# Optimization experiments

Measured on AMD Instinct MI355X. Metric: run time of the kernel, lower is better.

The kernel has to match this reference:

```python
import jax, jax.numpy as jnp
import numpy as np

N = 384       # nodes
K = 60        # neighbors per node
SUB = 20      # subsample_k
C_S = 128
C_Z = 128
H = 4
D_HEAD = C_Z // H
NUM_RBF = 64
E = N * K
EPS = 1e-8


def _rbf(D, D_min=0.0, D_max=20.0, D_count=NUM_RBF):
    # radial basis expansion of distances: [..., ] -> [..., D_count]
    mu = jnp.linspace(D_min, D_max, D_count)
    sigma = (D_max - D_min) / D_count
    return jnp.exp(-(((D[..., None] - mu) / sigma) ** 2))


def setup_inputs() -> dict:
    key = jax.random.key(0)
    ks = jax.random.split(key, 16)
    f32 = jnp.float32
    inp = {
        "node_features": jax.random.normal(ks[0], (N, C_S), f32),
        "node_trans": jax.random.normal(ks[1], (N, 3), f32) * 5.0,
        "edge_features": jax.random.normal(ks[2], (E, C_Z), f32),
        "edge_index": jax.random.randint(ks[3], (2, E), 0, N),
        "subsample_idx": jax.random.randint(ks[4], (N, K, SUB), 0, K),
        # dist_bias_gate: Linear(2*c_s -> H)
        "W_gate": jax.random.normal(ks[5], (2 * C_S, H), f32) / np.sqrt(2 * C_S),
        "b_gate": jnp.zeros((H,), f32),
        # dist_bias: Linear(num_rbf -> H)
        "W_db": jax.random.normal(ks[6], (NUM_RBF, H), f32) / np.sqrt(NUM_RBF),
        "b_db": jnp.zeros((H,), f32),
        # lin_qk: Linear(c_z -> 2*c_z)
        "W_qk": jax.random.normal(ks[7], (C_Z, 2 * C_Z), f32) / np.sqrt(C_Z),
        "b_qk": jnp.zeros((2 * C_Z,), f32),
        # lin_v: Linear(c_z -> c_z)
        "W_v": jax.random.normal(ks[8], (C_Z, C_Z), f32) / np.sqrt(C_Z),
        "b_v": jnp.zeros((C_Z,), f32),
        # lin_out: Linear(c_z -> c_z) (init='final' in source; random here for testing)
        "W_out": jax.random.normal(ks[9], (C_Z, C_Z), f32) / np.sqrt(C_Z),
        "b_out": jnp.zeros((C_Z,), f32),
    }
    return inp


def reference(node_features, node_trans, edge_features, edge_index, subsample_idx,
              W_gate, b_gate, W_db, b_db, W_qk, b_qk, W_v, b_v, W_out, b_out):
    n, k, sub = subsample_idx.shape
    # assume_sorted=True path: edges are grouped k-per-destination-node
    dst = edge_index[0].reshape(n, k)                           # [n,k] neighbor ids
    edge1 = jnp.broadcast_to(dst[:, :, None], (n, k, sub))      # [n,k,sub]
    edge2 = jnp.take_along_axis(
        jnp.broadcast_to(dst[:, None, :], (n, k, k)), subsample_idx, axis=-1)  # [n,k,sub]

    f1 = node_features[edge1]                                   # [n,k,sub,c_s]
    f2 = node_features[edge2]
    gate = jax.nn.sigmoid(jnp.concatenate([f1, f2], axis=-1) @ W_gate + b_gate)  # [n,k,sub,H]

    t1 = node_trans[edge1]                                      # [n,k,sub,3]
    t2 = node_trans[edge2]
    dist = jnp.linalg.norm(t1 - t2 + EPS, axis=-1)              # [n,k,sub]
    bias = gate * (_rbf(dist) @ W_db + b_db)                    # [n,k,sub,H]

    edges = edge_features.reshape(n, k, C_Z)
    qk = edges @ W_qk + b_qk
    q, kk = jnp.split(qk, 2, axis=-1)
    q = q.reshape(n, k, H, D_HEAD)
    kk = kk.reshape(n, k, H, D_HEAD)

    batch = jnp.arange(n)[:, None, None]
    k_sub = kk[batch, subsample_idx]                            # [n,k,sub,H,d]
    attn = jnp.einsum('nkhd,nkshd->nksh', q, k_sub) / np.sqrt(C_Z) + bias
    attn = jax.nn.softmax(attn, axis=2)                         # softmax over subsample axis

    v = (edges @ W_v + b_v).reshape(n, k, H, D_HEAD)
    v_sub = v[batch, subsample_idx]                             # [n,k,sub,H,d]
    upd = jnp.einsum('nksh,nkshd->nkhd', attn, v_sub).reshape(n * k, C_Z)
    return upd @ W_out + b_out                                  # [E, c_z]
```

## Files before the change

### kernel.cpp

```cpp
#include <hip/hip_runtime.h>
#include <hip/hip_bf16.h>

typedef unsigned short ushortT;
typedef __attribute__((ext_vector_type(8))) short bf16x8;
typedef __attribute__((ext_vector_type(4))) float f32x4;

#define N_NODES 384
#define KNBR 60
#define SUBK 20
#define NEDGE (N_NODES * KNBR)
#define EPSC 1e-8f
#define INV_SQRT_CZ 0.08838834764831845f
#define MU_STEP (20.0f / 63.0f)
#define INV_MU_STEP (63.0f / 20.0f)
#define INV_SIGMA 3.2f

__device__ __forceinline__ float bflo(unsigned int u) { return __uint_as_float(u << 16); }
__device__ __forceinline__ float bfhi(unsigned int u) { return __uint_as_float(u & 0xffff0000u); }
__device__ __forceinline__ ushortT f2bu(float v) {
  union { float f; unsigned int u; } c;
  c.f = v;
  return (ushortT)((c.u + 0x7fffu + ((c.u >> 16) & 1u)) >> 16);
}
__device__ __forceinline__ unsigned int pack2bf(float x, float y) {
  return (unsigned int)f2bu(x) | ((unsigned int)f2bu(y) << 16);
}
__device__ __forceinline__ ushortT f2h(float x) {
  _Float16 h = (_Float16)x;
  return __builtin_bit_cast(ushortT, h);
}
__device__ __forceinline__ float h2f(ushortT u) {
  return (float)__builtin_bit_cast(_Float16, u);
}

__global__ __launch_bounds__(256) void prep_kernel(
    const float* __restrict__ nf, const float* __restrict__ Wg, float* __restrict__ g,
    const float* __restrict__ Wqk, const float* __restrict__ bqk,
    const float* __restrict__ Wv, const float* __restrict__ bv,
    const float* __restrict__ Wout,
    ushortT* __restrict__ Wp1, ushortT* __restrict__ Wp2, float* __restrict__ bc) {
  int b = blockIdx.x, tid = threadIdx.x;
  if (b < 96) {
    int n = b * 4 + (tid >> 6), t = tid & 63;
    float a = nf[n * 128 + t];
    float bb = nf[n * 128 + 64 + t];
    float acc[8];
#pragma unroll
    for (int h = 0; h < 4; ++h) {
      acc[h]     = a * Wg[t * 4 + h]         + bb * Wg[(t + 64) * 4 + h];
      acc[4 + h] = a * Wg[(128 + t) * 4 + h] + bb * Wg[(192 + t) * 4 + h];
    }
#pragma unroll
    for (int i = 0; i < 8; ++i)
#pragma unroll
      for (int off = 32; off >= 1; off >>= 1) acc[i] += __shfl_xor(acc[i], off, 64);
    if (t == 0) {
#pragma unroll
      for (int i = 0; i < 8; ++i) g[n * 8 + i] = acc[i];
    }
  } else {
    int i = (b - 96) * 256 + tid;
    if (i < 49152) {
      int j = i & 7, l = (i >> 3) & 63, t = (i >> 9) & 3;
      int nt = (i >> 11) % 12, ny = (i >> 11) / 12;
      int nn = ny * 192 + nt * 16 + (l & 15);
      int k = t * 32 + (l >> 4) * 8 + j;
      float v = (nn < 256) ? Wqk[k * 256 + nn] : Wv[k * 128 + (nn - 256)];
      Wp1[i] = f2bu(v);
    } else {
      int i2 = i - 49152;
      int j = i2 & 7, l = (i2 >> 3) & 63, t = (i2 >> 9) & 3, nt = (i2 >> 11);
      int nn = nt * 16 + (l & 15);
      int k = t * 32 + (l >> 4) * 8 + j;
      Wp2[i2] = f2bu(Wout[k * 128 + nn]);
    }
    if (i < 384) bc[i] = (i < 256) ? bqk[i] : bv[i - 256];
  }
}

__global__ __launch_bounds__(256) void fused_kernel(
    const float* __restrict__ ef, const ushortT* __restrict__ Wp1,
    const ushortT* __restrict__ Wp2, const float* __restrict__ bc,
    const float* __restrict__ bout, const float* __restrict__ g,
    const float* __restrict__ node_trans, const int* __restrict__ edge_index,
    const int* __restrict__ sub_idx, const float* __restrict__ W_db,
    const float* __restrict__ b_db, const float* __restrict__ b_gate,
    float* __restrict__ outp) {
  __shared__ __align__(16) ushortT kvb[KNBR * 256];
  __shared__ __align__(16) ushortT updq[64 * 136];
  __shared__ __align__(16) ushortT unionb[4800];
  __shared__ ushortT sub_lds[KNBR * SUBK];
  __shared__ float trs[KNBR * 3];
  __shared__ float gg[KNBR * 8];
  __shared__ __align__(16) float wdb_lds[256];

  int n = blockIdx.x, tid = threadIdx.x;
  int e0 = n * KNBR;
  int w = tid >> 6, l = tid & 63;
  int lr = l & 15, lc = l >> 4;
  int row = w * 16 + lr;
  int rowc = min(row, KNBR - 1);

  wdb_lds[tid] = W_db[tid];
  if (tid < KNBR) {
    int dst = edge_index[e0 + tid];
#pragma unroll
    for (int c = 0; c < 3; ++c) trs[tid * 3 + c] = node_trans[dst * 3 + c];
#pragma unroll
    for (int i = 0; i < 8; ++i) gg[tid * 8 + i] = g[dst * 8 + i];
  }
  bf16x8 afrag[4];
#pragma unroll
  for (int t = 0; t < 4; ++t) {
    const float* ap = ef + (size_t)(e0 + rowc) * 128 + t * 32 + lc * 8;
    float4 lo = *(const float4*)ap;
    float4 hi = *(const float4*)(ap + 4);
    bf16x8 a;
    a[0] = (short)f2bu(lo.x); a[1] = (short)f2bu(lo.y);
    a[2] = (short)f2bu(lo.z); a[3] = (short)f2bu(lo.w);
    a[4] = (short)f2bu(hi.x); a[5] = (short)f2bu(hi.y);
    a[6] = (short)f2bu(hi.z); a[7] = (short)f2bu(hi.w);
    afrag[t] = a;
  }

  ushortT* Bb0 = unionb;
  ushortT* Bb1 = unionb + 2048;
  {
    uint4 p = *(const uint4*)(Wp1 + tid * 8);
    *(uint4*)(Bb0 + tid * 8) = p;
  }
  __syncthreads();

  float qv[32];
#pragma unroll
  for (int T = 0; T < 24; ++T) {
    if (T < 23) {
      uint4 p = *(const uint4*)(Wp1 + (T + 1) * 2048 + tid * 8);
      *(uint4*)(((T & 1) ? Bb0 : Bb1) + tid * 8) = p;
    }
    const ushortT* bb = (T & 1) ? Bb1 : Bb0;
    f32x4 acc = {0.f, 0.f, 0.f, 0.f};
#pragma unroll
    for (int t = 0; t < 4; ++t) {
      bf16x8 bfrag = *(const bf16x8*)(bb + (t * 64 + l) * 8);
      acc = __builtin_amdgcn_mfma_f32_16x16x32_bf16(bfrag, afrag[t], acc, 0, 0, 0);
    }
    int col0 = T * 16 + lc * 4;
    float4 bi = *(const float4*)(bc + col0);
    if (T < 8) {
      qv[T * 4 + 0] = (acc[0] + bi.x) * INV_SQRT_CZ;
      qv[T * 4 + 1] = (acc[1] + bi.y) * INV_SQRT_CZ;
      qv[T * 4 + 2] = (acc[2] + bi.z) * INV_SQRT_CZ;
      qv[T * 4 + 3] = (acc[3] + bi.w) * INV_SQRT_CZ;
    } else if (row < KNBR) {
      uint2 o;
      o.x = pack2bf(acc[0] + bi.x, acc[1] + bi.y);
      o.y = pack2bf(acc[2] + bi.z, acc[3] + bi.w);
      int byteoff = ((col0 - 128) * 2) ^ ((row & 7) << 4);
      *(uint2*)((char*)kvb + row * 512 + byteoff) = o;
    }
    __syncthreads();
  }
#pragma unroll
  for (int t = 0; t < 8; ++t) {
    uint2 o;
    o.x = pack2bf(qv[t * 4 + 0], qv[t * 4 + 1]);
    o.y = pack2bf(qv[t * 4 + 2], qv[t * 4 + 3]);
    *(uint2*)(updq + row * 136 + t * 16 + lc * 4) = o;
  }

  ushortT* biasb = unionb;
  float4 bgv = *(const float4*)b_gate;
  float4 bdbv = *(const float4*)b_db;
  for (int p = tid; p < KNBR * SUBK; p += 256) {
    int kl = p / SUBK, s = p - kl * SUBK;
    int j = sub_idx[(size_t)(e0 + kl) * SUBK + s];
    sub_lds[p] = (ushortT)j;
    float dx = trs[kl * 3 + 0] - trs[j * 3 + 0] + EPSC;
    float dy = trs[kl * 3 + 1] - trs[j * 3 + 1] + EPSC;
    float dz = trs[kl * 3 + 2] - trs[j * 3 + 2] + EPSC;
    float dist = sqrtf(dx * dx + dy * dy + dz * dz);
    int r0 = (int)(dist * INV_MU_STEP + 0.5f);
    int rlo = max(r0 - 4, 0), rhi = min(r0 + 4, 63);
    float a0 = 0.f, a1 = 0.f, a2 = 0.f, a3 = 0.f;
    for (int r = rlo; r <= rhi; ++r) {
      float t = (dist - r * MU_STEP) * INV_SIGMA;
      float e = __expf(-t * t);
      float4 wv = ((const float4*)wdb_lds)[r];
      a0 += e * wv.x; a1 += e * wv.y; a2 += e * wv.z; a3 += e * wv.w;
    }
    float g1 = gg[kl * 8 + 0] + gg[j * 8 + 4 + 0] + bgv.x;
    float g2 = gg[kl * 8 + 1] + gg[j * 8 + 4 + 1] + bgv.y;
    float g3 = gg[kl * 8 + 2] + gg[j * 8 + 4 + 2] + bgv.z;
    float g4 = gg[kl * 8 + 3] + gg[j * 8 + 4 + 3] + bgv.w;
    biasb[p * 4 + 0] = f2h((a0 + bdbv.x) / (1.0f + __expf(-g1)));
    biasb[p * 4 + 1] = f2h((a1 + bdbv.y) / (1.0f + __expf(-g2)));
    biasb[p * 4 + 2] = f2h((a2 + bdbv.z) / (1.0f + __expf(-g3)));
    biasb[p * 4 + 3] = f2h((a3 + bdbv.w) / (1.0f + __expf(-g4)));
  }
  __syncthreads();

  const char* kvbase = (const char*)kvb;
  float qh[32];
#pragma unroll
  for (int c = 0; c < 4; ++c) {
    uint4 u = *(const uint4*)(updq + row * 136 + lc * 32 + c * 8);
    qh[c * 8 + 0] = bflo(u.x); qh[c * 8 + 1] = bfhi(u.x);
    qh[c * 8 + 2] = bflo(u.y); qh[c * 8 + 3] = bfhi(u.y);
    qh[c * 8 + 4] = bflo(u.z); qh[c * 8 + 5] = bfhi(u.z);
    qh[c * 8 + 6] = bflo(u.w); qh[c * 8 + 7] = bfhi(u.w);
  }
  float logit[SUBK];
#pragma unroll
  for (int s = 0; s < SUBK; ++s) {
    int j = sub_lds[rowc * SUBK + s];
    int sw = (j & 7) << 4;
    float dot = 0.f;
#pragma unroll
    for (int c = 0; c < 4; ++c) {
      uint4 u = *(const uint4*)(kvbase + j * 512 + ((lc * 64 + c * 16) ^ sw));
      dot += qh[c * 8 + 0] * bflo(u.x) + qh[c * 8 + 1] * bfhi(u.x) +
             qh[c * 8 + 2] * bflo(u.y) + qh[c * 8 + 3] * bfhi(u.y) +
             qh[c * 8 + 4] * bflo(u.z) + qh[c * 8 + 5] * bfhi(u.z) +
             qh[c * 8 + 6] * bflo(u.w) + qh[c * 8 + 7] * bfhi(u.w);
    }
    logit[s] = dot + h2f(biasb[(rowc * SUBK + s) * 4 + lc]);
  }
  float m = logit[0];
#pragma unroll
  for (int s = 1; s < SUBK; ++s) m = fmaxf(m, logit[s]);
  float den = 0.f;
#pragma unroll
  for (int s = 0; s < SUBK; ++s) {
    logit[s] = __expf(logit[s] - m);
    den += logit[s];
  }
  float inv = 1.0f / den;
  float vacc[32];
#pragma unroll
  for (int i = 0; i < 32; ++i) vacc[i] = 0.f;
#pragma unroll
  for (int s = 0; s < SUBK; ++s) {
    int j = sub_lds[rowc * SUBK + s];
    int sw = (j & 7) << 4;
    float wgt = logit[s];
#pragma unroll
    for (int c = 0; c < 4; ++c) {
      uint4 u = *(const uint4*)(kvbase + j * 512 + ((256 + lc * 64 + c * 16) ^ sw));
      vacc[c * 8 + 0] += wgt * bflo(u.x); vacc[c * 8 + 1] += wgt * bfhi(u.x);
      vacc[c * 8 + 2] += wgt * bflo(u.y); vacc[c * 8 + 3] += wgt * bfhi(u.y);
      vacc[c * 8 + 4] += wgt * bflo(u.z); vacc[c * 8 + 5] += wgt * bfhi(u.z);
      vacc[c * 8 + 6] += wgt * bflo(u.w); vacc[c * 8 + 7] += wgt * bfhi(u.w);
    }
  }
#pragma unroll
  for (int c = 0; c < 4; ++c) {
    uint4 o;
    o.x = pack2bf(vacc[c * 8 + 0] * inv, vacc[c * 8 + 1] * inv);
    o.y = pack2bf(vacc[c * 8 + 2] * inv, vacc[c * 8 + 3] * inv);
    o.z = pack2bf(vacc[c * 8 + 4] * inv, vacc[c * 8 + 5] * inv);
    o.w = pack2bf(vacc[c * 8 + 6] * inv, vacc[c * 8 + 7] * inv);
    *(uint4*)(updq + row * 136 + lc * 32 + c * 8) = o;
  }
  __syncthreads();

  bf16x8 af2[4];
#pragma unroll
  for (int t = 0; t < 4; ++t)
    af2[t] = *(const bf16x8*)(updq + row * 136 + t * 32 + lc * 8);
  {
    uint4 p = *(const uint4*)(Wp2 + tid * 8);
    *(uint4*)(Bb0 + tid * 8) = p;
  }
  __syncthreads();
#pragma unroll
  for (int T = 0; T < 8; ++T) {
    if (T < 7) {
      uint4 p = *(const uint4*)(Wp2 + (T + 1) * 2048 + tid * 8);
      *(uint4*)(((T & 1) ? Bb0 : Bb1) + tid * 8) = p;
    }
    const ushortT* bb = (T & 1) ? Bb1 : Bb0;
    f32x4 acc = {0.f, 0.f, 0.f, 0.f};
#pragma unroll
    for (int t = 0; t < 4; ++t) {
      bf16x8 bfrag = *(const bf16x8*)(bb + (t * 64 + l) * 8);
      acc = __builtin_amdgcn_mfma_f32_16x16x32_bf16(bfrag, af2[t], acc, 0, 0, 0);
    }
    if (row < KNBR) {
      int col0 = T * 16 + lc * 4;
      float4 bi = *(const float4*)(bout + col0);
      float4 o;
      o.x = acc[0] + bi.x; o.y = acc[1] + bi.y;
      o.z = acc[2] + bi.z; o.w = acc[3] + bi.w;
      *(float4*)(outp + (size_t)(e0 + row) * 128 + col0) = o;
    }
    __syncthreads();
  }
}

extern "C" void kernel_launch(void* const* d_in, const int* in_sizes, int n_in, void* d_out,
                              int out_size, void* d_ws, size_t ws_size, hipStream_t stream) {
  const float* nf  = (const float*)d_in[0];
  const float* nt  = (const float*)d_in[1];
  const float* ef  = (const float*)d_in[2];
  const int*   ei  = (const int*)d_in[3];
  const int*   si  = (const int*)d_in[4];
  const float* Wg  = (const float*)d_in[5];
  const float* bg  = (const float*)d_in[6];
  const float* Wdb = (const float*)d_in[7];
  const float* bdb = (const float*)d_in[8];
  const float* Wqk = (const float*)d_in[9];
  const float* bqk = (const float*)d_in[10];
  const float* Wv  = (const float*)d_in[11];
  const float* bv  = (const float*)d_in[12];
  const float* Wout = (const float*)d_in[13];
  const float* bout = (const float*)d_in[14];
  float* out = (float*)d_out;

  float* g      = (float*)d_ws;
  float* bc     = g + 3072;
  ushortT* Wp1  = (ushortT*)(bc + 384);
  ushortT* Wp2  = Wp1 + 49152;

  prep_kernel<<<dim3(352), dim3(256), 0, stream>>>(nf, Wg, g, Wqk, bqk, Wv, bv, Wout,
                                                   Wp1, Wp2, bc);
  fused_kernel<<<dim3(N_NODES), dim3(256), 0, stream>>>(ef, Wp1, Wp2, bc, bout, g, nt, ei, si,
                                                        Wdb, bdb, bg, out);
}
```

Before: 45.84 us.

## Double block to 512 threads, split GEMM column tiles and attention heads

Launches 512 threads per node block. The two wave halves each compute half of the QKV and output GEMM column tiles. The B fragments now come straight from global memory instead of a double-buffered LDS staging area, which drops the per-tile barriers. The attention phase assigns one thread per (row, head, half-head) and combines partial dot products with a lane shuffle, cutting per-thread registers and raising parallelism. W_db is read from global rather than LDS. The cost is more redundant global and L2 reads of weights, plus a larger block size.

Result: faster. 40.20 us (-12.3%).

```diff
diff --git a/kernel.cpp b/kernel.cpp
--- a/kernel.cpp
+++ b/kernel.cpp
@@ -78,7 +78,7 @@
   }
 }
 
-__global__ __launch_bounds__(256) void fused_kernel(
+__global__ __launch_bounds__(512, 4) void fused_kernel(
     const float* __restrict__ ef, const ushortT* __restrict__ Wp1,
     const ushortT* __restrict__ Wp2, const float* __restrict__ bc,
     const float* __restrict__ bout, const float* __restrict__ g,
@@ -88,20 +88,18 @@
     float* __restrict__ outp) {
   __shared__ __align__(16) ushortT kvb[KNBR * 256];
   __shared__ __align__(16) ushortT updq[64 * 136];
-  __shared__ __align__(16) ushortT unionb[4800];
+  __shared__ __align__(16) ushortT biasb[KNBR * SUBK * 4];
   __shared__ ushortT sub_lds[KNBR * SUBK];
   __shared__ float trs[KNBR * 3];
   __shared__ float gg[KNBR * 8];
-  __shared__ __align__(16) float wdb_lds[256];
 
   int n = blockIdx.x, tid = threadIdx.x;
   int e0 = n * KNBR;
   int w = tid >> 6, l = tid & 63;
   int lr = l & 15, lc = l >> 4;
-  int row = w * 16 + lr;
-  int rowc = min(row, KNBR - 1);
-
-  wdb_lds[tid] = W_db[tid];
+  int rowA = (w & 3) * 16 + lr;
+  int rowAc = min(rowA, KNBR - 1);
+
   if (tid < KNBR) {
     int dst = edge_index[e0 + tid];
 #pragma unroll
@@ -112,7 +110,7 @@
   bf16x8 afrag[4];
 #pragma unroll
   for (int t = 0; t < 4; ++t) {
-    const float* ap = ef + (size_t)(e0 + rowc) * 128 + t * 32 + lc * 8;
+    const float* ap = ef + (size_t)(e0 + rowAc) * 128 + t * 32 + lc * 8;
     float4 lo = *(const float4*)ap;
     float4 hi = *(const float4*)(ap + 4);
     bf16x8 a;
@@ -123,56 +121,38 @@
     afrag[t] = a;
   }
 
-  ushortT* Bb0 = unionb;
-  ushortT* Bb1 = unionb + 2048;
-  {
-    uint4 p = *(const uint4*)(Wp1 + tid * 8);
-    *(uint4*)(Bb0 + tid * 8) = p;
-  }
-  __syncthreads();
-
-  float qv[32];
-#pragma unroll
-  for (int T = 0; T < 24; ++T) {
-    if (T < 23) {
-      uint4 p = *(const uint4*)(Wp1 + (T + 1) * 2048 + tid * 8);
-      *(uint4*)(((T & 1) ? Bb0 : Bb1) + tid * 8) = p;
-    }
-    const ushortT* bb = (T & 1) ? Bb1 : Bb0;
+  int Tbase = (tid >> 8) * 12;
+#pragma unroll
+  for (int Ti = 0; Ti < 12; ++Ti) {
+    int T = Tbase + Ti;
     f32x4 acc = {0.f, 0.f, 0.f, 0.f};
 #pragma unroll
     for (int t = 0; t < 4; ++t) {
-      bf16x8 bfrag = *(const bf16x8*)(bb + (t * 64 + l) * 8);
+      bf16x8 bfrag = *(const bf16x8*)(Wp1 + ((T * 4 + t) * 64 + l) * 8);
       acc = __builtin_amdgcn_mfma_f32_16x16x32_bf16(bfrag, afrag[t], acc, 0, 0, 0);
     }
     int col0 = T * 16 + lc * 4;
     float4 bi = *(const float4*)(bc + col0);
+    float o0 = acc[0] + bi.x, o1 = acc[1] + bi.y;
+    float o2 = acc[2] + bi.z, o3 = acc[3] + bi.w;
     if (T < 8) {
-      qv[T * 4 + 0] = (acc[0] + bi.x) * INV_SQRT_CZ;
-      qv[T * 4 + 1] = (acc[1] + bi.y) * INV_SQRT_CZ;
-      qv[T * 4 + 2] = (acc[2] + bi.z) * INV_SQRT_CZ;
-      qv[T * 4 + 3] = (acc[3] + bi.w) * INV_SQRT_CZ;
-    } else if (row < KNBR) {
       uint2 o;
-      o.x = pack2bf(acc[0] + bi.x, acc[1] + bi.y);
-      o.y = pack2bf(acc[2] + bi.z, acc[3] + bi.w);
-      int byteoff = ((col0 - 128) * 2) ^ ((row & 7) << 4);
-      *(uint2*)((char*)kvb + row * 512 + byteoff) = o;
-    }
-    __syncthreads();
-  }
-#pragma unroll
-  for (int t = 0; t < 8; ++t) {
-    uint2 o;
-    o.x = pack2bf(qv[t * 4 + 0], qv[t * 4 + 1]);
-    o.y = pack2bf(qv[t * 4 + 2], qv[t * 4 + 3]);
-    *(uint2*)(updq + row * 136 + t * 16 + lc * 4) = o;
-  }
-
-  ushortT* biasb = unionb;
+      o.x = pack2bf(o0 * INV_SQRT_CZ, o1 * INV_SQRT_CZ);
+      o.y = pack2bf(o2 * INV_SQRT_CZ, o3 * INV_SQRT_CZ);
+      *(uint2*)(updq + rowA * 136 + col0) = o;
+    } else if (rowA < KNBR) {
+      uint2 o;
+      o.x = pack2bf(o0, o1);
+      o.y = pack2bf(o2, o3);
+      int byteoff = ((col0 - 128) * 2) ^ ((rowA & 7) << 4);
+      *(uint2*)((char*)kvb + rowA * 512 + byteoff) = o;
+    }
+  }
+  __syncthreads();
+
   float4 bgv = *(const float4*)b_gate;
   float4 bdbv = *(const float4*)b_db;
-  for (int p = tid; p < KNBR * SUBK; p += 256) {
+  for (int p = tid; p < KNBR * SUBK; p += 512) {
     int kl = p / SUBK, s = p - kl * SUBK;
     int j = sub_idx[(size_t)(e0 + kl) * SUBK + s];
     sub_lds[p] = (ushortT)j;
@@ -186,7 +166,7 @@
     for (int r = rlo; r <= rhi; ++r) {
       float t = (dist - r * MU_STEP) * INV_SIGMA;
       float e = __expf(-t * t);
-      float4 wv = ((const float4*)wdb_lds)[r];
+      float4 wv = ((const float4*)W_db)[r];
       a0 += e * wv.x; a1 += e * wv.y; a2 += e * wv.z; a3 += e * wv.w;
     }
     float g1 = gg[kl * 8 + 0] + gg[j * 8 + 4 + 0] + bgv.x;
@@ -200,31 +180,35 @@
   }
   __syncthreads();
 
+  int row3 = tid >> 3, h = (tid >> 1) & 3, dh = tid & 1;
+  int row3c = min(row3, KNBR - 1);
   const char* kvbase = (const char*)kvb;
-  float qh[32];
-#pragma unroll
-  for (int c = 0; c < 4; ++c) {
-    uint4 u = *(const uint4*)(updq + row * 136 + lc * 32 + c * 8);
-    qh[c * 8 + 0] = bflo(u.x); qh[c * 8 + 1] = bfhi(u.x);
-    qh[c * 8 + 2] = bflo(u.y); qh[c * 8 + 3] = bfhi(u.y);
-    qh[c * 8 + 4] = bflo(u.z); qh[c * 8 + 5] = bfhi(u.z);
-    qh[c * 8 + 6] = bflo(u.w); qh[c * 8 + 7] = bfhi(u.w);
+  float qh[16];
+  {
+    const ushortT* qp = updq + row3 * 136 + h * 32 + dh * 16;
+    uint4 u0 = *(const uint4*)qp;
+    uint4 u1 = *(const uint4*)(qp + 8);
+    qh[0] = bflo(u0.x); qh[1] = bfhi(u0.x); qh[2] = bflo(u0.y); qh[3] = bfhi(u0.y);
+    qh[4] = bflo(u0.z); qh[5] = bfhi(u0.z); qh[6] = bflo(u0.w); qh[7] = bfhi(u0.w);
+    qh[8] = bflo(u1.x); qh[9] = bfhi(u1.x); qh[10] = bflo(u1.y); qh[11] = bfhi(u1.y);
+    qh[12] = bflo(u1.z); qh[13] = bfhi(u1.z); qh[14] = bflo(u1.w); qh[15] = bfhi(u1.w);
   }
   float logit[SUBK];
 #pragma unroll
   for (int s = 0; s < SUBK; ++s) {
-    int j = sub_lds[rowc * SUBK + s];
+    int j = sub_lds[row3c * SUBK + s];
     int sw = (j & 7) << 4;
     float dot = 0.f;
 #pragma unroll
-    for (int c = 0; c < 4; ++c) {
-      uint4 u = *(const uint4*)(kvbase + j * 512 + ((lc * 64 + c * 16) ^ sw));
+    for (int c = 0; c < 2; ++c) {
+      uint4 u = *(const uint4*)(kvbase + j * 512 + ((h * 64 + dh * 32 + c * 16) ^ sw));
       dot += qh[c * 8 + 0] * bflo(u.x) + qh[c * 8 + 1] * bfhi(u.x) +
              qh[c * 8 + 2] * bflo(u.y) + qh[c * 8 + 3] * bfhi(u.y) +
              qh[c * 8 + 4] * bflo(u.z) + qh[c * 8 + 5] * bfhi(u.z) +
              qh[c * 8 + 6] * bflo(u.w) + qh[c * 8 + 7] * bfhi(u.w);
     }
-    logit[s] = dot + h2f(biasb[(rowc * SUBK + s) * 4 + lc]);
+    dot += __shfl_xor(dot, 1);
+    logit[s] = dot + h2f(biasb[(row3c * SUBK + s) * 4 + h]);
   }
   float m = logit[0];
 #pragma unroll
@@ -236,17 +220,17 @@
     den += logit[s];
   }
   float inv = 1.0f / den;
-  float vacc[32];
-#pragma unroll
-  for (int i = 0; i < 32; ++i) vacc[i] = 0.f;
+  float vacc[16];
+#pragma unroll
+  for (int i = 0; i < 16; ++i) vacc[i] = 0.f;
 #pragma unroll
   for (int s = 0; s < SUBK; ++s) {
-    int j = sub_lds[rowc * SUBK + s];
+    int j = sub_lds[row3c * SUBK + s];
     int sw = (j & 7) << 4;
     float wgt = logit[s];
 #pragma unroll
-    for (int c = 0; c < 4; ++c) {
-      uint4 u = *(const uint4*)(kvbase + j * 512 + ((256 + lc * 64 + c * 16) ^ sw));
+    for (int c = 0; c < 2; ++c) {
+      uint4 u = *(const uint4*)(kvbase + j * 512 + ((256 + h * 64 + dh * 32 + c * 16) ^ sw));
       vacc[c * 8 + 0] += wgt * bflo(u.x); vacc[c * 8 + 1] += wgt * bfhi(u.x);
       vacc[c * 8 + 2] += wgt * bflo(u.y); vacc[c * 8 + 3] += wgt * bfhi(u.y);
       vacc[c * 8 + 4] += wgt * bflo(u.z); vacc[c * 8 + 5] += wgt * bfhi(u.z);
@@ -254,47 +238,38 @@
     }
   }
 #pragma unroll
-  for (int c = 0; c < 4; ++c) {
+  for (int c = 0; c < 2; ++c) {
     uint4 o;
     o.x = pack2bf(vacc[c * 8 + 0] * inv, vacc[c * 8 + 1] * inv);
     o.y = pack2bf(vacc[c * 8 + 2] * inv, vacc[c * 8 + 3] * inv);
     o.z = pack2bf(vacc[c * 8 + 4] * inv, vacc[c * 8 + 5] * inv);
     o.w = pack2bf(vacc[c * 8 + 6] * inv, vacc[c * 8 + 7] * inv);
-    *(uint4*)(updq + row * 136 + lc * 32 + c * 8) = o;
+    *(uint4*)(updq + row3 * 136 + h * 32 + dh * 16 + c * 8) = o;
   }
   __syncthreads();
 
   bf16x8 af2[4];
 #pragma unroll
   for (int t = 0; t < 4; ++t)
-    af2[t] = *(const bf16x8*)(updq + row * 136 + t * 32 + lc * 8);
-  {
-    uint4 p = *(const uint4*)(Wp2 + tid * 8);
-    *(uint4*)(Bb0 + tid * 8) = p;
-  }
-  __syncthreads();
-#pragma unroll
-  for (int T = 0; T < 8; ++T) {
-    if (T < 7) {
-      uint4 p = *(const uint4*)(Wp2 + (T + 1) * 2048 + tid * 8);
-      *(uint4*)(((T & 1) ? Bb0 : Bb1) + tid * 8) = p;
-    }
-    const ushortT* bb = (T & 1) ? Bb1 : Bb0;
+    af2[t] = *(const bf16x8*)(updq + rowA * 136 + t * 32 + lc * 8);
+  int T4base = (tid >> 8) * 4;
+#pragma unroll
+  for (int Ti = 0; Ti < 4; ++Ti) {
+    int T = T4base + Ti;
     f32x4 acc = {0.f, 0.f, 0.f, 0.f};
 #pragma unroll
     for (int t = 0; t < 4; ++t) {
-      bf16x8 bfrag = *(const bf16x8*)(bb + (t * 64 + l) * 8);
+      bf16x8 bfrag = *(const bf16x8*)(Wp2 + ((T * 4 + t) * 64 + l) * 8);
       acc = __builtin_amdgcn_mfma_f32_16x16x32_bf16(bfrag, af2[t], acc, 0, 0, 0);
     }
-    if (row < KNBR) {
+    if (rowA < KNBR) {
       int col0 = T * 16 + lc * 4;
       float4 bi = *(const float4*)(bout + col0);
       float4 o;
       o.x = acc[0] + bi.x; o.y = acc[1] + bi.y;
       o.z = acc[2] + bi.z; o.w = acc[3] + bi.w;
-      *(float4*)(outp + (size_t)(e0 + row) * 128 + col0) = o;
-    }
-    __syncthreads();
+      *(float4*)(outp + (size_t)(e0 + rowA) * 128 + col0) = o;
+    }
   }
 }
 
@@ -324,6 +299,6 @@
 
   prep_kernel<<<dim3(352), dim3(256), 0, stream>>>(nf, Wg, g, Wqk, bqk, Wv, bv, Wout,
                                                    Wp1, Wp2, bc);
-  fused_kernel<<<dim3(N_NODES), dim3(256), 0, stream>>>(ef, Wp1, Wp2, bc, bout, g, nt, ei, si,
+  fused_kernel<<<dim3(N_NODES), dim3(512), 0, stream>>>(ef, Wp1, Wp2, bc, bout, g, nt, ei, si,
                                                         Wdb, bdb, bg, out);
 }
```
